# Kernel tuning notes

Hardware: AMD Instinct MI355X
Metric: run time of the kernel (lower is better)

Reference implementation:

```python
import jax, jax.numpy as jnp
import numpy as np
from math import sqrt

H = 16
D_MODEL = 1024
D_K = D_MODEL // H
B, S = 2, 2048


def setup_inputs() -> dict:
    key = jax.random.key(0)
    ks = jax.random.split(key, 12)
    scale = 1.0 / sqrt(D_MODEL)
    inp = {
        "query": jax.random.normal(ks[0], (B, S, D_MODEL), jnp.float32),
        "key": jax.random.normal(ks[1], (B, S, D_MODEL), jnp.float32),
        "value": jax.random.normal(ks[2], (B, S, D_MODEL), jnp.float32),
        # causal mask [B, S, S]; module unsqueezes head dim itself
        "mask": jnp.broadcast_to(jnp.tril(jnp.ones((S, S), jnp.int32)), (B, S, S)),
        "Wq": jax.random.normal(ks[3], (D_MODEL, D_MODEL), jnp.float32) * scale,
        "bq": jnp.zeros((D_MODEL,), jnp.float32),
        "Wk": jax.random.normal(ks[4], (D_MODEL, D_MODEL), jnp.float32) * scale,
        "bk": jnp.zeros((D_MODEL,), jnp.float32),
        "Wv": jax.random.normal(ks[5], (D_MODEL, D_MODEL), jnp.float32) * scale,
        "bv": jnp.zeros((D_MODEL,), jnp.float32),
        "Wo": jax.random.normal(ks[6], (D_MODEL, D_MODEL), jnp.float32) * scale,
        "bo": jnp.zeros((D_MODEL,), jnp.float32),
    }
    return inp


def reference(query, key, value, mask, Wq, bq, Wk, bk, Wv, bv, Wo, bo):
    nb = query.shape[0]

    def proj(x, W, b):
        # nn.Linear: x @ W.T + b, then split heads -> [B, H, S, D_K]
        y = jnp.einsum('bsd,ed->bse', x, W) + b
        return y.reshape(nb, -1, H, D_K).transpose(0, 2, 1, 3)

    q = proj(query, Wq, bq)
    k = proj(key, Wk, bk)
    v = proj(value, Wv, bv)

    scores = jnp.einsum('bhqd,bhkd->bhqk', q, k) / sqrt(D_K)  # [B,H,S,S]
    scores = jnp.where(mask[:, None, :, :] == 0, -jnp.inf, scores)
    probs = jax.nn.softmax(scores, axis=-1)  # dropout in eval mode (identity)
    ctx = jnp.einsum('bhqk,bhkd->bhqd', probs, v)
    ctx = ctx.transpose(0, 2, 1, 3).reshape(nb, -1, H * D_K)
    return jnp.einsum('bsd,ed->bse', ctx, Wo) + bo
```

## Files before the change

### kernel.cpp

```cpp
#include <hip/hip_runtime.h>
#include <hip/hip_bf16.h>
#include <stdint.h>


#define H_ 16
#define DM 1024
#define DK_ 64
#define BB 2
#define SS 2048
#define PSTR 72

typedef __bf16 bf16x8 __attribute__((ext_vector_type(8)));
typedef __bf16 bf16x2_t __attribute__((ext_vector_type(2)));
typedef float f32x4 __attribute__((ext_vector_type(4)));

#define GLOAD_LDS16(g, l)                                            \
  __builtin_amdgcn_global_load_lds(                                  \
      (__attribute__((address_space(1))) void*)(g),                  \
      (__attribute__((address_space(3))) void*)(l), 16, 0, 0)

__device__ __forceinline__ unsigned short f2bf_u(float f) {
  unsigned int u = __float_as_uint(f);
  u += 0x7fffu + ((u >> 16) & 1u);
  return (unsigned short)(u >> 16);
}

__device__ __forceinline__ unsigned int pack_bf16(float a, float b) {
#if __has_builtin(__builtin_amdgcn_cvt_pk_bf16_f32)
  bf16x2_t v = __builtin_amdgcn_cvt_pk_bf16_f32(a, b);
  unsigned int u;
  __builtin_memcpy(&u, &v, 4);
  return u;
#else
  return (unsigned int)f2bf_u(a) | ((unsigned int)f2bf_u(b) << 16);
#endif
}

__device__ __forceinline__ float fexp2(float x) {
#if __has_builtin(__builtin_amdgcn_exp2f)
  return __builtin_amdgcn_exp2f(x);
#else
  return exp2f(x);
#endif
}

struct Cvt {
  const float* s[7];
  unsigned short* d[7];
  int n[7];
};

__global__ __launch_bounds__(256) void convert_kernel(Cvt c) {
  const int y = blockIdx.y;
  const float* __restrict__ src = c.s[y];
  unsigned short* __restrict__ dst = c.d[y];
  const int nv = c.n[y] >> 2;
  for (int i = blockIdx.x * 256 + threadIdx.x; i < nv; i += 1024 * 256) {
    float4 v = *(const float4*)(src + (size_t)i * 4);
    ushort4 o;
    o.x = f2bf_u(v.x); o.y = f2bf_u(v.y); o.z = f2bf_u(v.z); o.w = f2bf_u(v.w);
    *(ushort4*)(dst + (size_t)i * 4) = o;
  }
}

template <int TN>
__device__ __forceinline__ void gemm_dbuf(
    const unsigned short* __restrict__ A, const unsigned short* __restrict__ W,
    unsigned short* As, unsigned short* Bs, int m0, int n0,
    f32x4 (*acc)[TN / 32]) {
  constexpr int FW = TN / 32;
  const int tid = threadIdx.x;
  const int wave = tid >> 6, lane = tid & 63;
  const int lm = lane & 15, quad = lane >> 4;
  const int wm = (wave >> 1) * 64, wn = (wave & 1) * (16 * FW);
  const int srow = lane >> 2;
  const int scol = (lane & 3) * 8;

#pragma unroll
  for (int i = 0; i < 4; ++i)
#pragma unroll
    for (int j = 0; j < FW; ++j) {
      f32x4 z = {0.f, 0.f, 0.f, 0.f};
      acc[i][j] = z;
    }

#pragma unroll
  for (int cc = 0; cc < 2; ++cc) {
    int c = wave * 2 + cc;
    GLOAD_LDS16(A + (size_t)(m0 + c * 16 + srow) * DM + scol,
                As + c * 512 + lane * 8);
  }
  if (TN == 128) {
#pragma unroll
    for (int cc = 0; cc < 2; ++cc) {
      int c = wave * 2 + cc;
      GLOAD_LDS16(W + (size_t)(n0 + c * 16 + srow) * DM + scol,
                  Bs + c * 512 + lane * 8);
    }
  } else {
    GLOAD_LDS16(W + (size_t)(n0 + wave * 16 + srow) * DM + scol,
                Bs + wave * 512 + lane * 8);
  }

  for (int kt = 0; kt < DM / 32; ++kt) {
    __syncthreads();
    const int cur = kt & 1;
    const unsigned short* Ac = As + cur * (128 * 32);
    const unsigned short* Bc = Bs + cur * (TN * 32);
    if (kt + 1 < DM / 32) {
      unsigned short* An = As + (cur ^ 1) * (128 * 32);
      unsigned short* Bn = Bs + (cur ^ 1) * (TN * 32);
      const int kcol = (kt + 1) * 32 + scol;
#pragma unroll
      for (int cc = 0; cc < 2; ++cc) {
        int c = wave * 2 + cc;
        GLOAD_LDS16(A + (size_t)(m0 + c * 16 + srow) * DM + kcol,
                    An + c * 512 + lane * 8);
      }
      if (TN == 128) {
#pragma unroll
        for (int cc = 0; cc < 2; ++cc) {
          int c = wave * 2 + cc;
          GLOAD_LDS16(W + (size_t)(n0 + c * 16 + srow) * DM + kcol,
                      Bn + c * 512 + lane * 8);
        }
      } else {
        GLOAD_LDS16(W + (size_t)(n0 + wave * 16 + srow) * DM + kcol,
                    Bn + wave * 512 + lane * 8);
      }
    }
    bf16x8 af[4], bfr[FW];
#pragma unroll
    for (int i = 0; i < 4; ++i)
      af[i] = *(const bf16x8*)(Ac + (wm + i * 16 + lm) * 32 + quad * 8);
#pragma unroll
    for (int j = 0; j < FW; ++j)
      bfr[j] = *(const bf16x8*)(Bc + (wn + j * 16 + lm) * 32 + quad * 8);
#pragma unroll
    for (int i = 0; i < 4; ++i)
#pragma unroll
      for (int j = 0; j < FW; ++j)
        acc[i][j] = __builtin_amdgcn_mfma_f32_16x16x32_bf16(af[i], bfr[j],
                                                            acc[i][j], 0, 0, 0);
  }
}

__global__ __launch_bounds__(512, 2) void qkv_gemm(
    const unsigned short* Qi, const unsigned short* Ki, const unsigned short* Vi,
    const unsigned short* Wq, const unsigned short* Wk, const unsigned short* Wv,
    const float* bq, const float* bk, const float* bv,
    unsigned short* Qf, unsigned short* Kf, unsigned short* Vf) {
  __shared__ unsigned short As[2 * 2 * 16 * 512];
  __shared__ unsigned short Bs[2 * 2 * 16 * 512];
  const int p = blockIdx.x;
  const int c = p & 7, idx = p >> 3;
  const int x = idx & 3, yy = (idx >> 2) & 1, z = idx >> 3;
  const int y = c * 2 + yy;
  const int m0 = y * 256, n0 = x * 256;
  const unsigned short* A = z == 0 ? Qi : (z == 1 ? Ki : Vi);
  const unsigned short* W = z == 0 ? Wq : (z == 1 ? Wk : Wv);
  const float* bias = z == 0 ? bq : (z == 1 ? bk : bv);
  const float scale = z == 0 ? 0.1803368801111204f : 1.0f;

  const int tid = threadIdx.x;
  const int wave = tid >> 6, lane = tid & 63;
  const int lm = lane & 15, quad = lane >> 4;
  const int wr = wave >> 2, wc = wave & 3;

  const int scs = 8 * ((lane & 3) ^ ((lane >> 3) & 3));
  const size_t asrc0 = (size_t)(m0 + wave * 16 + (lane >> 2)) * DM + scs;
  const size_t bsrc0 = (size_t)(n0 + wave * 16 + (lane >> 2)) * DM + scs;
  const int sdst = wave * 512 + lane * 8;

  const int rcol = (quad * 8) ^ (((lm >> 1) & 3) * 8);
  const int aoff = wr * 8 * 512 + lm * 32 + rcol;
  const int boff = wc * 4 * 512 + lm * 32 + rcol;

  f32x4 acc[8][4];
#pragma unroll
  for (int i = 0; i < 8; ++i)
#pragma unroll
    for (int j = 0; j < 4; ++j) {
      f32x4 zz = {0.f, 0.f, 0.f, 0.f};
      acc[i][j] = zz;
    }

  auto stA = [&](int buf, int kh, int kt) {
    const unsigned short* s = A + asrc0 + (size_t)kt * 64 + kh * 32;
    unsigned short* d = As + buf * 16384 + kh * 8192 + sdst;
    GLOAD_LDS16(s, d);
    GLOAD_LDS16(s + (size_t)128 * DM, d + 4096);
  };
  auto stB = [&](int buf, int kh, int kt) {
    const unsigned short* s = W + bsrc0 + (size_t)kt * 64 + kh * 32;
    unsigned short* d = Bs + buf * 16384 + kh * 8192 + sdst;
    GLOAD_LDS16(s, d);
    GLOAD_LDS16(s + (size_t)128 * DM, d + 4096);
  };

  stA(0, 0, 0); stB(0, 0, 0); stA(0, 1, 0); stB(0, 1, 0);
  stA(1, 0, 1); stB(1, 0, 1); stA(1, 1, 1);
  asm volatile("s_waitcnt vmcnt(6)" ::: "memory");
  __builtin_amdgcn_s_barrier();

#define BARR __builtin_amdgcn_s_barrier()
#define SCHB __builtin_amdgcn_sched_barrier(0)
#define MFMA8(AF, B0_, B1_, J0, J1)                                          \
  __builtin_amdgcn_s_setprio(1);                                             \
  _Pragma("unroll")                                                          \
  for (int i = 0; i < 8; ++i) {                                              \
    acc[i][J0] = __builtin_amdgcn_mfma_f32_16x16x32_bf16(AF[i], B0_,         \
                                                         acc[i][J0], 0, 0, 0); \
    acc[i][J1] = __builtin_amdgcn_mfma_f32_16x16x32_bf16(AF[i], B1_,         \
                                                         acc[i][J1], 0, 0, 0); \
  }                                                                          \
  __builtin_amdgcn_s_setprio(0)

#pragma unroll 2
  for (int t = 0; t < 14; ++t) {
    const int buf = t & 1;
    const unsigned short* Ab = As + buf * 16384;
    const unsigned short* Bb = Bs + buf * 16384;
    bf16x8 a0[8], b0[4];
#pragma unroll
    for (int i = 0; i < 8; ++i)
      a0[i] = *(const bf16x8*)(Ab + aoff + i * 512);
#pragma unroll
    for (int j = 0; j < 4; ++j)
      b0[j] = *(const bf16x8*)(Bb + boff + j * 512);
    stB(buf ^ 1, 1, t + 1);
    BARR; SCHB;
    MFMA8(a0, b0[0], b0[1], 0, 1);
    SCHB; BARR;
    stA(buf, 0, t + 2);
    BARR; SCHB;
    MFMA8(a0, b0[2], b0[3], 2, 3);
    SCHB; BARR;
    bf16x8 a1[8], b1[4];
#pragma unroll
    for (int i = 0; i < 8; ++i)
      a1[i] = *(const bf16x8*)(Ab + 8192 + aoff + i * 512);
#pragma unroll
    for (int j = 0; j < 4; ++j)
      b1[j] = *(const bf16x8*)(Bb + 8192 + boff + j * 512);
    stB(buf, 0, t + 2);
    BARR; SCHB;
    MFMA8(a1, b1[0], b1[1], 0, 1);
    SCHB; BARR;
    stA(buf, 1, t + 2);
    asm volatile("s_waitcnt vmcnt(6)" ::: "memory");
    BARR; SCHB;
    MFMA8(a1, b1[2], b1[3], 2, 3);
    SCHB; BARR;
  }

  stB(1, 1, 15);
  asm volatile("s_waitcnt vmcnt(0)" ::: "memory");
  __builtin_amdgcn_s_barrier();
#pragma unroll
  for (int tt = 0; tt < 2; ++tt) {
    const unsigned short* Ab = As + tt * 16384;
    const unsigned short* Bb = Bs + tt * 16384;
#pragma unroll
    for (int kh = 0; kh < 2; ++kh) {
      bf16x8 a2[8], b2[4];
#pragma unroll
      for (int i = 0; i < 8; ++i)
        a2[i] = *(const bf16x8*)(Ab + kh * 8192 + aoff + i * 512);
#pragma unroll
      for (int j = 0; j < 4; ++j)
        b2[j] = *(const bf16x8*)(Bb + kh * 8192 + boff + j * 512);
#pragma unroll
      for (int i = 0; i < 8; ++i)
#pragma unroll
        for (int j = 0; j < 4; ++j)
          acc[i][j] = __builtin_amdgcn_mfma_f32_16x16x32_bf16(
              a2[i], b2[j], acc[i][j], 0, 0, 0);
    }
  }
#undef MFMA8
#undef SCHB
#undef BARR

  if (z == 2) {
#pragma unroll
    for (int j = 0; j < 4; ++j) {
      int gn = n0 + wc * 64 + j * 16 + lm;
      float bv_ = bias[gn];
      int h2 = gn >> 6, dk = gn & 63;
      int a = dk >> 4, ln = dk & 15;
#pragma unroll
      for (int i = 0; i < 8; ++i) {
        int s0 = m0 + wr * 128 + i * 16 + quad * 4;
        int b2 = s0 >> 11, sl = s0 & 2047;
        int kt2 = sl >> 6, cc2 = (sl >> 5) & 1, qk = (sl >> 3) & 3, j0 = sl & 7;
        size_t base =
            ((size_t)(((b2 * 16 + h2) * 32 + kt2) * 4 + a) * 2 + cc2) * 512 +
            (qk * 16 + ln) * 8 + j0;
        uint2 w;
        w.x = pack_bf16(acc[i][j][0] + bv_, acc[i][j][1] + bv_);
        w.y = pack_bf16(acc[i][j][2] + bv_, acc[i][j][3] + bv_);
        *(uint2*)(Vf + base) = w;
      }
    }
  } else {
    unsigned short* out = z == 0 ? Qf : Kf;
#pragma unroll
    for (int j = 0; j < 4; ++j) {
      int gn = n0 + wc * 64 + j * 16 + lm;
      float bv_ = bias[gn];
      int h2 = gn >> 6, d64 = gn & 63;
      int cc2 = (d64 >> 5) & 1, qk = (d64 >> 3) & 3, jjq = d64 & 7;
#pragma unroll
      for (int i = 0; i < 8; ++i)
#pragma unroll
        for (int r = 0; r < 4; ++r) {
          int gm = m0 + wr * 128 + i * 16 + quad * 4 + r;
          int b2 = gm >> 11, sl = gm & 2047;
          size_t base =
              ((size_t)((b2 * 16 + h2) * 128 + (sl >> 4)) * 2 + cc2) * 512 +
              (qk * 16 + (sl & 15)) * 8 + jjq;
          out[base] = f2bf_u((acc[i][j][r] + bv_) * scale);
        }
    }
  }
}

__global__ __launch_bounds__(256) void o_gemm(
    const unsigned short* Ctx, const unsigned short* Wo, const float* bo,
    float* out) {
  __shared__ unsigned short As[2 * 128 * 32], Bs[2 * 64 * 32];
  const int p = blockIdx.x;
  const int c = p & 7, j0 = p >> 3;
  const int x = j0 & 15, yy = j0 >> 4;
  const int y = c * 4 + yy;
  const int m0 = y * 128, n0 = x * 64;
  f32x4 acc[4][2];
  gemm_dbuf<64>(Ctx, Wo, As, Bs, m0, n0, acc);
  const int lane = threadIdx.x & 63, wave = threadIdx.x >> 6;
  const int lm = lane & 15, quad = lane >> 4;
  const int wm = (wave >> 1) * 64, wn = (wave & 1) * 32;
#pragma unroll
  for (int j = 0; j < 2; ++j) {
    int gn = n0 + wn + j * 16 + lm;
    float bv_ = bo[gn];
#pragma unroll
    for (int i = 0; i < 4; ++i)
#pragma unroll
      for (int r = 0; r < 4; ++r) {
        int gm = m0 + wm + i * 16 + quad * 4 + r;
        out[(size_t)gm * DM + gn] = acc[i][j][r] + bv_;
      }
  }
}

__global__ __launch_bounds__(256, 2) void attn_kernel(
    const unsigned short* __restrict__ Qf, const unsigned short* __restrict__ Kf,
    const unsigned short* __restrict__ Vf, unsigned short* __restrict__ Ctx) {
  __shared__ unsigned short Ps[4][16 * PSTR];
  const int p = blockIdx.x;
  const int bh = p & 31, pr = p >> 5;
  const int b = bh >> 4, h = bh & 15;
  const int tid = threadIdx.x, wave = tid >> 6, lane = tid & 63;
  const int lm = lane & 15, quad = lane >> 4;

  const unsigned short* Kb = Kf + (size_t)bh * 256 * 512;
  const unsigned short* Vb = Vf + (size_t)bh * 256 * 512;
  unsigned short* Pw = Ps[wave];

  bf16x8 onesf;
  {
    unsigned short ob[8] = {0x3F80, 0x3F80, 0x3F80, 0x3F80,
                            0x3F80, 0x3F80, 0x3F80, 0x3F80};
    __builtin_memcpy(&onesf, ob, 16);
  }

  auto loadK = [&](bf16x8 (&kf)[4][2], int kt) {
#pragma unroll
    for (int ik = 0; ik < 4; ++ik)
#pragma unroll
      for (int c = 0; c < 2; ++c)
        kf[ik][c] = *(const bf16x8*)(Kb +
            ((size_t)(kt * 4 + ik) * 2 + c) * 512 + lane * 8);
  };
  auto loadV = [&](bf16x8 (&vf)[4][2], int kt) {
#pragma unroll
    for (int a = 0; a < 4; ++a)
#pragma unroll
      for (int c = 0; c < 2; ++c)
        vf[a][c] = *(const bf16x8*)(Vb +
            ((size_t)(kt * 8 + a * 2 + c)) * 512 + lane * 8);
  };

  for (int pass = 0; pass < 2; ++pass) {
    const int qb = pass ? 31 - pr : pr;
    const int qbase = qb * 64 + wave * 16;
    const int nkw = qb + 1;

    bf16x8 qf[2];
#pragma unroll
    for (int c = 0; c < 2; ++c)
      qf[c] = *(const bf16x8*)(Qf +
          ((size_t)(bh * 128 + (qbase >> 4)) * 2 + c) * 512 + lane * 8);

    f32x4 oacc[4];
#pragma unroll
    for (int a = 0; a < 4; ++a) {
      f32x4 z = {0.f, 0.f, 0.f, 0.f};
      oacc[a] = z;
    }
    f32x4 lacc = {0.f, 0.f, 0.f, 0.f};

    auto compute = [&](bf16x8 (&kf)[4][2], bf16x8 (&vf)[4][2], int kt,
                       bool last) {
      f32x4 s[4];
#pragma unroll
      for (int ik = 0; ik < 4; ++ik) {
        f32x4 zz = {0.f, 0.f, 0.f, 0.f};
        zz = __builtin_amdgcn_mfma_f32_16x16x32_bf16(kf[ik][0], qf[0], zz,
                                                     0, 0, 0);
        s[ik] = __builtin_amdgcn_mfma_f32_16x16x32_bf16(kf[ik][1], qf[1], zz,
                                                        0, 0, 0);
      }
      if (last) {
#pragma unroll
        for (int ik = 0; ik < 4; ++ik)
#pragma unroll
          for (int r = 0; r < 4; ++r) {
            int kg = kt * 64 + ik * 16 + quad * 4 + r;
            int qg = qbase + lm;
            if (kg > qg) s[ik][r] = -1e30f;
          }
      }
#pragma unroll
      for (int ik = 0; ik < 4; ++ik) {
        float p0 = fexp2(s[ik][0]);
        float p1 = fexp2(s[ik][1]);
        float p2 = fexp2(s[ik][2]);
        float p3 = fexp2(s[ik][3]);
        uint2 w;
        w.x = pack_bf16(p0, p1);
        w.y = pack_bf16(p2, p3);
        *(uint2*)(Pw + lm * PSTR + ik * 16 + quad * 4) = w;
      }
      bf16x8 pf[2];
#pragma unroll
      for (int c = 0; c < 2; ++c)
        pf[c] = *(const bf16x8*)(Pw + lm * PSTR + c * 32 + quad * 8);
#pragma unroll
      for (int a = 0; a < 4; ++a) {
        oacc[a] = __builtin_amdgcn_mfma_f32_16x16x32_bf16(pf[0], vf[a][0],
                                                          oacc[a], 0, 0, 0);
        oacc[a] = __builtin_amdgcn_mfma_f32_16x16x32_bf16(pf[1], vf[a][1],
                                                          oacc[a], 0, 0, 0);
      }
      lacc = __builtin_amdgcn_mfma_f32_16x16x32_bf16(pf[0], onesf, lacc,
                                                     0, 0, 0);
      lacc = __builtin_amdgcn_mfma_f32_16x16x32_bf16(pf[1], onesf, lacc,
                                                     0, 0, 0);
    };

    bf16x8 kA[4][2], vA[4][2], kB[4][2], vB[4][2];
    loadK(kA, 0);
    loadV(vA, 0);
    for (int kt = 0; kt < nkw; kt += 2) {
      if (kt + 1 < nkw) { loadK(kB, kt + 1); loadV(vB, kt + 1); }
      compute(kA, vA, kt, kt == nkw - 1);
      if (kt + 1 < nkw) {
        if (kt + 2 < nkw) { loadK(kA, kt + 2); loadV(vA, kt + 2); }
        compute(kB, vB, kt + 1, kt + 1 == nkw - 1);
      }
    }

#pragma unroll
    for (int r = 0; r < 4; ++r) {
      float inv = 1.0f / lacc[r];
      int qg = qbase + quad * 4 + r;
#pragma unroll
      for (int a = 0; a < 4; ++a)
        Ctx[(size_t)(b * SS + qg) * DM + h * DK_ + a * 16 + lm] =
            f2bf_u(oacc[a][r] * inv);
    }
  }
}

extern "C" void kernel_launch(void* const* d_in, const int* in_sizes, int n_in,
                              void* d_out, int out_size, void* d_ws, size_t ws_size,
                              hipStream_t stream) {
  const float* q = (const float*)d_in[0];
  const float* k = (const float*)d_in[1];
  const float* v = (const float*)d_in[2];
  const float* Wq = (const float*)d_in[4];
  const float* bq = (const float*)d_in[5];
  const float* Wk = (const float*)d_in[6];
  const float* bk = (const float*)d_in[7];
  const float* Wv = (const float*)d_in[8];
  const float* bv = (const float*)d_in[9];
  const float* Wo = (const float*)d_in[10];
  const float* bo = (const float*)d_in[11];

  const size_t NX = (size_t)BB * SS * DM;
  const size_t NW = (size_t)DM * DM;
  unsigned short* ws = (unsigned short*)d_ws;
  unsigned short* Qi = ws;
  unsigned short* Ki = Qi + NX;
  unsigned short* Vi = Ki + NX;
  unsigned short* Wqb = Vi + NX;
  unsigned short* Wkb = Wqb + NW;
  unsigned short* Wvb = Wkb + NW;
  unsigned short* Wob = Wvb + NW;
  unsigned short* Qfr = Wob + NW;
  unsigned short* Kfr = Qfr + NX;
  unsigned short* Vfr = Kfr + NX;
  unsigned short* Ctx = Vfr + NX;

  Cvt c;
  c.s[0] = q; c.s[1] = k; c.s[2] = v; c.s[3] = Wq; c.s[4] = Wk; c.s[5] = Wv; c.s[6] = Wo;
  c.d[0] = Qi; c.d[1] = Ki; c.d[2] = Vi; c.d[3] = Wqb; c.d[4] = Wkb; c.d[5] = Wvb; c.d[6] = Wob;
  c.n[0] = c.n[1] = c.n[2] = (int)NX;
  c.n[3] = c.n[4] = c.n[5] = c.n[6] = (int)NW;

  convert_kernel<<<dim3(1024, 7), dim3(256), 0, stream>>>(c);
  qkv_gemm<<<dim3(192), dim3(512), 0, stream>>>(Qi, Ki, Vi, Wqb, Wkb, Wvb,
                                                bq, bk, bv, Qfr, Kfr, Vfr);
  attn_kernel<<<dim3(512), dim3(256), 0, stream>>>(Qfr, Kfr, Vfr, Ctx);
  o_gemm<<<dim3(512), dim3(256), 0, stream>>>(Ctx, Wob, bo, (float*)d_out);
}
```

Baseline: 233.8 us.

## Stage K/V tiles through LDS via async global_load_lds double buffering

Each wave previously loaded the full K and V tiles from global memory into registers, so all four waves fetched the same data. Now the block cooperatively stages each K/V tile into double-buffered shared memory with global_load_lds, and waves read fragments from LDS. This cuts redundant global/L2 traffic and register pressure, at the cost of a block-wide barrier on every key tile and extra LDS reads.

```diff
diff --git a/kernel.cpp b/kernel.cpp
--- a/kernel.cpp
+++ b/kernel.cpp
@@ -357,6 +357,8 @@
 __global__ __launch_bounds__(256, 2) void attn_kernel(
     const unsigned short* __restrict__ Qf, const unsigned short* __restrict__ Kf,
     const unsigned short* __restrict__ Vf, unsigned short* __restrict__ Ctx) {
+  __shared__ unsigned short Ks[2][8 * 512];
+  __shared__ unsigned short Vs[2][8 * 512];
   __shared__ unsigned short Ps[4][16 * PSTR];
   const int p = blockIdx.x;
   const int bh = p & 31, pr = p >> 5;
@@ -375,21 +377,15 @@
     __builtin_memcpy(&onesf, ob, 16);
   }
 
-  auto loadK = [&](bf16x8 (&kf)[4][2], int kt) {
-#pragma unroll
-    for (int ik = 0; ik < 4; ++ik)
-#pragma unroll
-      for (int c = 0; c < 2; ++c)
-        kf[ik][c] = *(const bf16x8*)(Kb +
-            ((size_t)(kt * 4 + ik) * 2 + c) * 512 + lane * 8);
-  };
-  auto loadV = [&](bf16x8 (&vf)[4][2], int kt) {
-#pragma unroll
-    for (int a = 0; a < 4; ++a)
-#pragma unroll
-      for (int c = 0; c < 2; ++c)
-        vf[a][c] = *(const bf16x8*)(Vb +
-            ((size_t)(kt * 8 + a * 2 + c)) * 512 + lane * 8);
+  auto stage = [&](int buf, int kt) {
+#pragma unroll
+    for (int cc = 0; cc < 2; ++cc) {
+      int ch = wave * 2 + cc;
+      GLOAD_LDS16(Kb + ((size_t)kt * 8 + ch) * 512 + lane * 8,
+                  &Ks[buf][ch * 512 + lane * 8]);
+      GLOAD_LDS16(Vb + ((size_t)kt * 8 + ch) * 512 + lane * 8,
+                  &Vs[buf][ch * 512 + lane * 8]);
+    }
   };
 
   for (int pass = 0; pass < 2; ++pass) {
@@ -411,18 +407,26 @@
     }
     f32x4 lacc = {0.f, 0.f, 0.f, 0.f};
 
-    auto compute = [&](bf16x8 (&kf)[4][2], bf16x8 (&vf)[4][2], int kt,
-                       bool last) {
+    __syncthreads();
+    stage(0, 0);
+
+    for (int kt = 0; kt < nkw; ++kt) {
+      __syncthreads();
+      const int buf = kt & 1;
+      if (kt + 1 < nkw) stage(buf ^ 1, kt + 1);
+
+      const unsigned short* Kc = Ks[buf];
+      const unsigned short* Vc = Vs[buf];
       f32x4 s[4];
 #pragma unroll
       for (int ik = 0; ik < 4; ++ik) {
+        bf16x8 k0 = *(const bf16x8*)(Kc + (ik * 2 + 0) * 512 + lane * 8);
+        bf16x8 k1 = *(const bf16x8*)(Kc + (ik * 2 + 1) * 512 + lane * 8);
         f32x4 zz = {0.f, 0.f, 0.f, 0.f};
-        zz = __builtin_amdgcn_mfma_f32_16x16x32_bf16(kf[ik][0], qf[0], zz,
-                                                     0, 0, 0);
-        s[ik] = __builtin_amdgcn_mfma_f32_16x16x32_bf16(kf[ik][1], qf[1], zz,
-                                                        0, 0, 0);
-      }
-      if (last) {
+        zz = __builtin_amdgcn_mfma_f32_16x16x32_bf16(k0, qf[0], zz, 0, 0, 0);
+        s[ik] = __builtin_amdgcn_mfma_f32_16x16x32_bf16(k1, qf[1], zz, 0, 0, 0);
+      }
+      if (kt == nkw - 1) {
 #pragma unroll
         for (int ik = 0; ik < 4; ++ik)
 #pragma unroll
@@ -449,27 +453,17 @@
         pf[c] = *(const bf16x8*)(Pw + lm * PSTR + c * 32 + quad * 8);
 #pragma unroll
       for (int a = 0; a < 4; ++a) {
-        oacc[a] = __builtin_amdgcn_mfma_f32_16x16x32_bf16(pf[0], vf[a][0],
+        bf16x8 v0 = *(const bf16x8*)(Vc + (a * 2 + 0) * 512 + lane * 8);
+        bf16x8 v1 = *(const bf16x8*)(Vc + (a * 2 + 1) * 512 + lane * 8);
+        oacc[a] = __builtin_amdgcn_mfma_f32_16x16x32_bf16(pf[0], v0,
                                                           oacc[a], 0, 0, 0);
-        oacc[a] = __builtin_amdgcn_mfma_f32_16x16x32_bf16(pf[1], vf[a][1],
+        oacc[a] = __builtin_amdgcn_mfma_f32_16x16x32_bf16(pf[1], v1,
                                                           oacc[a], 0, 0, 0);
       }
       lacc = __builtin_amdgcn_mfma_f32_16x16x32_bf16(pf[0], onesf, lacc,
                                                      0, 0, 0);
       lacc = __builtin_amdgcn_mfma_f32_16x16x32_bf16(pf[1], onesf, lacc,
                                                      0, 0, 0);
-    };
-
-    bf16x8 kA[4][2], vA[4][2], kB[4][2], vB[4][2];
-    loadK(kA, 0);
-    loadV(vA, 0);
-    for (int kt = 0; kt < nkw; kt += 2) {
-      if (kt + 1 < nkw) { loadK(kB, kt + 1); loadV(vB, kt + 1); }
-      compute(kA, vA, kt, kt == nkw - 1);
-      if (kt + 1 < nkw) {
-        if (kt + 2 < nkw) { loadK(kA, kt + 2); loadV(vA, kt + 2); }
-        compute(kB, vB, kt + 1, kt + 1 == nkw - 1);
-      }
     }
 
 #pragma unroll
```

Measured after the change: 231.1 us. About the same (-1.2%).

## Split attention KV range across waves with LDS reduction, one q-tile per block

Applied to the files above, without the earlier changes.

Restructures the attention kernel so each block handles a single 64-row query tile, and its four waves split the key/value tiles among themselves (split-K), each computing partial outputs and row sums for all 64 query rows. The partials are combined through a shared-memory reduction before normalization and storing. The grid doubles to 1024 blocks, with heaviest tiles scheduled first, replacing the two-pass causal pairing. This trades more register pressure (4x accumulators and Q fragments), the removed register double-buffering of K/V, and a reduction epilogue with barriers for better parallelism and shared K/V reuse across query rows.

```diff
diff --git a/kernel.cpp b/kernel.cpp
--- a/kernel.cpp
+++ b/kernel.cpp
@@ -357,12 +357,16 @@
 __global__ __launch_bounds__(256, 2) void attn_kernel(
     const unsigned short* __restrict__ Qf, const unsigned short* __restrict__ Kf,
     const unsigned short* __restrict__ Vf, unsigned short* __restrict__ Ctx) {
+  __shared__ float Rs[4][64][21];
   __shared__ unsigned short Ps[4][16 * PSTR];
   const int p = blockIdx.x;
-  const int bh = p & 31, pr = p >> 5;
+  const int bh = p & 31, qt = 31 - (p >> 5);
   const int b = bh >> 4, h = bh & 15;
   const int tid = threadIdx.x, wave = tid >> 6, lane = tid & 63;
   const int lm = lane & 15, quad = lane >> 4;
+
+  const int qbase0 = qt * 64;
+  const int nkw = qt + 1;
 
   const unsigned short* Kb = Kf + (size_t)bh * 256 * 512;
   const unsigned short* Vb = Vf + (size_t)bh * 256 * 512;
@@ -375,60 +379,63 @@
     __builtin_memcpy(&onesf, ob, 16);
   }
 
-  auto loadK = [&](bf16x8 (&kf)[4][2], int kt) {
+  bf16x8 qf[4][2];
+#pragma unroll
+  for (int f = 0; f < 4; ++f)
+#pragma unroll
+    for (int c = 0; c < 2; ++c)
+      qf[f][c] = *(const bf16x8*)(Qf +
+          ((size_t)(bh * 128 + qt * 4 + f) * 2 + c) * 512 + lane * 8);
+
+  f32x4 oacc[4][4];
+#pragma unroll
+  for (int f = 0; f < 4; ++f)
+#pragma unroll
+    for (int a = 0; a < 4; ++a) {
+      f32x4 z = {0.f, 0.f, 0.f, 0.f};
+      oacc[f][a] = z;
+    }
+  f32x4 lacc[4];
+#pragma unroll
+  for (int f = 0; f < 4; ++f) {
+    f32x4 z = {0.f, 0.f, 0.f, 0.f};
+    lacc[f] = z;
+  }
+
+  for (int kt = wave; kt < nkw; kt += 4) {
+    bf16x8 kf[4][2], vf[4][2];
 #pragma unroll
     for (int ik = 0; ik < 4; ++ik)
 #pragma unroll
       for (int c = 0; c < 2; ++c)
         kf[ik][c] = *(const bf16x8*)(Kb +
             ((size_t)(kt * 4 + ik) * 2 + c) * 512 + lane * 8);
-  };
-  auto loadV = [&](bf16x8 (&vf)[4][2], int kt) {
 #pragma unroll
     for (int a = 0; a < 4; ++a)
 #pragma unroll
       for (int c = 0; c < 2; ++c)
         vf[a][c] = *(const bf16x8*)(Vb +
             ((size_t)(kt * 8 + a * 2 + c)) * 512 + lane * 8);
-  };
-
-  for (int pass = 0; pass < 2; ++pass) {
-    const int qb = pass ? 31 - pr : pr;
-    const int qbase = qb * 64 + wave * 16;
-    const int nkw = qb + 1;
-
-    bf16x8 qf[2];
-#pragma unroll
-    for (int c = 0; c < 2; ++c)
-      qf[c] = *(const bf16x8*)(Qf +
-          ((size_t)(bh * 128 + (qbase >> 4)) * 2 + c) * 512 + lane * 8);
-
-    f32x4 oacc[4];
-#pragma unroll
-    for (int a = 0; a < 4; ++a) {
-      f32x4 z = {0.f, 0.f, 0.f, 0.f};
-      oacc[a] = z;
-    }
-    f32x4 lacc = {0.f, 0.f, 0.f, 0.f};
-
-    auto compute = [&](bf16x8 (&kf)[4][2], bf16x8 (&vf)[4][2], int kt,
-                       bool last) {
+    const bool last = (kt == nkw - 1);
+
+#pragma unroll
+    for (int f = 0; f < 4; ++f) {
       f32x4 s[4];
 #pragma unroll
       for (int ik = 0; ik < 4; ++ik) {
         f32x4 zz = {0.f, 0.f, 0.f, 0.f};
-        zz = __builtin_amdgcn_mfma_f32_16x16x32_bf16(kf[ik][0], qf[0], zz,
+        zz = __builtin_amdgcn_mfma_f32_16x16x32_bf16(kf[ik][0], qf[f][0], zz,
                                                      0, 0, 0);
-        s[ik] = __builtin_amdgcn_mfma_f32_16x16x32_bf16(kf[ik][1], qf[1], zz,
-                                                        0, 0, 0);
+        s[ik] = __builtin_amdgcn_mfma_f32_16x16x32_bf16(kf[ik][1], qf[f][1],
+                                                        zz, 0, 0, 0);
       }
       if (last) {
+        int qg = qbase0 + f * 16 + lm;
 #pragma unroll
         for (int ik = 0; ik < 4; ++ik)
 #pragma unroll
           for (int r = 0; r < 4; ++r) {
             int kg = kt * 64 + ik * 16 + quad * 4 + r;
-            int qg = qbase + lm;
             if (kg > qg) s[ik][r] = -1e30f;
           }
       }
@@ -449,37 +456,39 @@
         pf[c] = *(const bf16x8*)(Pw + lm * PSTR + c * 32 + quad * 8);
 #pragma unroll
       for (int a = 0; a < 4; ++a) {
-        oacc[a] = __builtin_amdgcn_mfma_f32_16x16x32_bf16(pf[0], vf[a][0],
-                                                          oacc[a], 0, 0, 0);
-        oacc[a] = __builtin_amdgcn_mfma_f32_16x16x32_bf16(pf[1], vf[a][1],
-                                                          oacc[a], 0, 0, 0);
-      }
-      lacc = __builtin_amdgcn_mfma_f32_16x16x32_bf16(pf[0], onesf, lacc,
-                                                     0, 0, 0);
-      lacc = __builtin_amdgcn_mfma_f32_16x16x32_bf16(pf[1], onesf, lacc,
-                                                     0, 0, 0);
-    };
-
-    bf16x8 kA[4][2], vA[4][2], kB[4][2], vB[4][2];
-    loadK(kA, 0);
-    loadV(vA, 0);
-    for (int kt = 0; kt < nkw; kt += 2) {
-      if (kt + 1 < nkw) { loadK(kB, kt + 1); loadV(vB, kt + 1); }
-      compute(kA, vA, kt, kt == nkw - 1);
-      if (kt + 1 < nkw) {
-        if (kt + 2 < nkw) { loadK(kA, kt + 2); loadV(vA, kt + 2); }
-        compute(kB, vB, kt + 1, kt + 1 == nkw - 1);
-      }
-    }
-
+        oacc[f][a] = __builtin_amdgcn_mfma_f32_16x16x32_bf16(pf[0], vf[a][0],
+                                                             oacc[f][a], 0, 0, 0);
+        oacc[f][a] = __builtin_amdgcn_mfma_f32_16x16x32_bf16(pf[1], vf[a][1],
+                                                             oacc[f][a], 0, 0, 0);
+      }
+      lacc[f] = __builtin_amdgcn_mfma_f32_16x16x32_bf16(pf[0], onesf, lacc[f],
+                                                        0, 0, 0);
+      lacc[f] = __builtin_amdgcn_mfma_f32_16x16x32_bf16(pf[1], onesf, lacc[f],
+                                                        0, 0, 0);
+    }
+  }
+
+  const size_t obase = (size_t)(b * SS) * DM + (size_t)h * DK_;
+#pragma unroll
+  for (int f = 0; f < 4; ++f) {
+    __syncthreads();
+#pragma unroll
+    for (int a = 0; a < 4; ++a)
+#pragma unroll
+      for (int r = 0; r < 4; ++r)
+        Rs[wave][lane][a * 4 + r] = oacc[f][a][r];
+#pragma unroll
+    for (int r = 0; r < 4; ++r)
+      Rs[wave][lane][16 + r] = lacc[f][r];
+    __syncthreads();
 #pragma unroll
     for (int r = 0; r < 4; ++r) {
-      float inv = 1.0f / lacc[r];
-      int qg = qbase + quad * 4 + r;
-#pragma unroll
-      for (int a = 0; a < 4; ++a)
-        Ctx[(size_t)(b * SS + qg) * DM + h * DK_ + a * 16 + lm] =
-            f2bf_u(oacc[a][r] * inv);
+      float ov = Rs[0][lane][wave * 4 + r] + Rs[1][lane][wave * 4 + r] +
+                 Rs[2][lane][wave * 4 + r] + Rs[3][lane][wave * 4 + r];
+      float lv = Rs[0][lane][16 + r] + Rs[1][lane][16 + r] +
+                 Rs[2][lane][16 + r] + Rs[3][lane][16 + r];
+      int qg = qbase0 + f * 16 + quad * 4 + r;
+      Ctx[obase + (size_t)qg * DM + wave * 16 + lm] = f2bf_u(ov / lv);
     }
   }
 }
@@ -523,6 +532,6 @@
   convert_kernel<<<dim3(1024, 7), dim3(256), 0, stream>>>(c);
   qkv_gemm<<<dim3(192), dim3(512), 0, stream>>>(Qi, Ki, Vi, Wqb, Wkb, Wvb,
                                                 bq, bk, bv, Qfr, Kfr, Vfr);
-  attn_kernel<<<dim3(512), dim3(256), 0, stream>>>(Qfr, Kfr, Vfr, Ctx);
+  attn_kernel<<<dim3(1024), dim3(256), 0, stream>>>(Qfr, Kfr, Vfr, Ctx);
   o_gemm<<<dim3(512), dim3(256), 0, stream>>>(Ctx, Wob, bo, (float*)d_out);
 }
```

Result: faster. 228.3 us (-2.4%).
